# Optimization experiments

Measured on AMD Instinct MI355X. Metric: run time of the kernel, lower is better.

The kernel has to match this reference:

```python
import jax, jax.numpy as jnp
import numpy as np

B, S, D, H, F = 2, 2048, 768, 12, 3072
HD = D // H


def setup_inputs() -> dict:
    key = jax.random.key(0)
    ks = jax.random.split(key, 6)
    g = lambda k, sh, sc: jax.random.normal(k, sh, jnp.float32) * sc
    return {
        "x": g(ks[0], (B, S, D), 1.0),
        "mask": jnp.tril(jnp.ones((1, 1, S, S), dtype=jnp.bool_)),  # causal
        "qkv_w": g(ks[1], (3 * D, D), 0.02),
        "qkv_b": jnp.zeros((3 * D,), jnp.float32),
        "out_w": g(ks[2], (D, D), 0.02),
        "out_b": jnp.zeros((D,), jnp.float32),
        "fc1_w": g(ks[3], (F, D), 0.02),
        "fc1_b": jnp.zeros((F,), jnp.float32),
        "fc2_w": g(ks[4], (D, F), 0.02),
        "fc2_b": jnp.zeros((D,), jnp.float32),
        "ln1_w": jnp.ones((D,), jnp.float32),
        "ln1_b": jnp.zeros((D,), jnp.float32),
        "ln2_w": jnp.ones((D,), jnp.float32),
        "ln2_b": jnp.zeros((D,), jnp.float32),
    }


def _layernorm(x, w, b, eps=1e-5):
    m = x.mean(-1, keepdims=True)
    v = ((x - m) ** 2).mean(-1, keepdims=True)
    return (x - m) * jax.lax.rsqrt(v + eps) * w + b


def reference(x, mask, qkv_w, qkv_b, out_w, out_b, fc1_w, fc1_b, fc2_w, fc2_b,
              ln1_w, ln1_b, ln2_w, ln2_b):
    b, s, d = x.shape
    h = d // HD  # num_heads
    # --- pre-norm multi-head self-attention (dropout = eval/identity) ---
    hx = _layernorm(x, ln1_w, ln1_b)
    qkv = hx @ qkv_w.T + qkv_b                      # [b,s,3d]
    qkv = qkv.reshape(b, s, 3, h, HD).transpose(2, 0, 3, 1, 4)  # [3,b,h,s,hd]
    q, k, v = qkv[0], qkv[1], qkv[2]
    scale = jnp.sqrt(jnp.float32(HD))
    scores = jnp.einsum("bhqd,bhkd->bhqk", q, k) / scale  # [b,h,s,s]
    scores = jnp.where(mask, scores, -jnp.inf)
    attn = jax.nn.softmax(scores, axis=-1)
    o = jnp.einsum("bhqk,bhkd->bhqd", attn, v)      # [b,h,s,hd]
    o = o.transpose(0, 2, 1, 3).reshape(b, s, d)
    x = x + (o @ out_w.T + out_b)
    # --- pre-norm GELU feed-forward ---
    h2 = _layernorm(x, ln2_w, ln2_b)
    ff = jax.nn.gelu(h2 @ fc1_w.T + fc1_b, approximate=False) @ fc2_w.T + fc2_b
    return x + ff
```

## Files before the change

### kernel.cpp

```cpp
#include <hip/hip_runtime.h>
#include <hip/hip_bf16.h>
#include <cstdint>
#include <cstddef>

typedef __bf16 bf16;
typedef unsigned short ushort_t;
typedef __attribute__((ext_vector_type(8))) __bf16 bf16x8;
typedef __attribute__((ext_vector_type(4))) __bf16 bf16x4;
typedef __attribute__((ext_vector_type(4))) float f32x4;

#define NB 2
#define NS 2048
#define ND 768
#define NH 12
#define NF 3072
#define NT (NB * NS)

__device__ __forceinline__ f32x4 mfma16(bf16x8 a, bf16x8 b, f32x4 c) {
  return __builtin_amdgcn_mfma_f32_16x16x32_bf16(a, b, c, 0, 0, 0);
}

__device__ __forceinline__ void gl_lds16(const bf16* g, bf16* l) {
  __builtin_amdgcn_global_load_lds(
      (__attribute__((address_space(1))) void*)(uintptr_t)g,
      (__attribute__((address_space(3))) void*)l,
      16, 0, 0);
}

__device__ __forceinline__ int xcd_swz(int lin, int nwg) {
  const int q = nwg >> 3, r = nwg & 7;
  const int x = lin & 7, i = lin >> 3;
  return (x < r ? x * (q + 1) : r * (q + 1) + (x - r) * q) + i;
}

__device__ __forceinline__ float gelu_fast(float v) {
  const float u = v * (0.7978845608028654f + 0.03567740814f * v * v);
  const float e = exp2f(u * 2.885390081777927f);
  return v - v / (1.f + e);
}

__global__ __launch_bounds__(256) void sniff_kernel(
    const ushort_t* __restrict__ x, int* __restrict__ flag) {
  __shared__ int s[4];
  int bad = 0;
  for (int i = threadIdx.x; i < 4096; i += 256) {
    const int e = (x[i] >> 7) & 0xFF;
    bad |= (e >= 0xC0);
  }
  bad = __any(bad) ? 1 : 0;
  if ((threadIdx.x & 63) == 0) s[threadIdx.x >> 6] = bad;
  __syncthreads();
  if (threadIdx.x == 0) *flag = s[0] | s[1] | s[2] | s[3];
}

struct CvtArgs {
  const void* s[8];
  bf16* d[8];
  int n8[8];
  int total8;
};

__global__ __launch_bounds__(256) void cvt_all(CvtArgs a,
                                               const int* __restrict__ flag) {
  const int isf = *flag;
  const int stride = gridDim.x * 256;
  for (int i = blockIdx.x * 256 + threadIdx.x; i < a.total8; i += stride) {
    int seg = 0, off = i;
    while (off >= a.n8[seg]) { off -= a.n8[seg]; ++seg; }
    bf16x8 o;
    if (isf) {
      const float* s = (const float*)a.s[seg] + (size_t)off * 8;
      const f32x4 f0 = *(const f32x4*)s;
      const f32x4 f1 = *(const f32x4*)(s + 4);
#pragma unroll
      for (int j = 0; j < 4; ++j) {
        o[j] = (bf16)f0[j];
        o[4 + j] = (bf16)f1[j];
      }
    } else {
      o = *((const bf16x8*)a.s[seg] + off);
    }
    *((bf16x8*)a.d[seg] + off) = o;
  }
}

__global__ __launch_bounds__(256) void ln_kernel(
    const void* __restrict__ xv, const void* __restrict__ wv,
    const void* __restrict__ bv, bf16* __restrict__ y,
    const int* __restrict__ flag) {
  const int isf = *flag;
  const int row = blockIdx.x * 4 + (threadIdx.x >> 6);
  const int L = threadIdx.x & 63;
  const float* xf = (const float*)xv;
  const bf16* xh = (const bf16*)xv;
  const float* wf = (const float*)wv;
  const bf16* wh = (const bf16*)wv;
  const float* bf_ = (const float*)bv;
  const bf16* bh = (const bf16*)bv;
  const size_t base = (size_t)row * ND;
  float v[12];
  float s = 0.f, s2 = 0.f;
#pragma unroll
  for (int i = 0; i < 12; ++i) {
    const int c = L + i * 64;
    v[i] = isf ? xf[base + c] : (float)xh[base + c];
    s += v[i];
    s2 += v[i] * v[i];
  }
#pragma unroll
  for (int off = 1; off < 64; off <<= 1) {
    s += __shfl_xor(s, off);
    s2 += __shfl_xor(s2, off);
  }
  const float mean = s * (1.f / 768.f);
  const float var = s2 * (1.f / 768.f) - mean * mean;
  const float rstd = rsqrtf(var + 1e-5f);
  bf16* yr = y + base;
#pragma unroll
  for (int i = 0; i < 12; ++i) {
    const int c = L + i * 64;
    const float ww = isf ? wf[c] : (float)wh[c];
    const float bb = isf ? bf_[c] : (float)bh[c];
    yr[c] = (bf16)((v[i] - mean) * rstd * ww + bb);
  }
}

__global__ __launch_bounds__(256) void vt_kernel(
    const bf16* __restrict__ qkv, bf16* __restrict__ vT) {
  const int bh = blockIdx.y;
  const int b = bh / NH, h = bh % NH;
  const int st = blockIdx.x;
  __shared__ bf16 Vs[64 * 72];
  const int tid = threadIdx.x;
  {
    const int r = tid >> 2, c = (tid & 3) * 16;
    const bf16* src =
        qkv + (size_t)(b * NS + st * 64 + r) * (3 * ND) + 2 * ND + h * 64 + c;
    *(bf16x8*)&Vs[r * 72 + c] = *(const bf16x8*)src;
    *(bf16x8*)&Vs[r * 72 + c + 8] = *(const bf16x8*)(src + 8);
  }
  __syncthreads();
  {
    const int hd = tid >> 2, t0 = (tid & 3) * 16;
    bf16x8 o0, o1;
#pragma unroll
    for (int j = 0; j < 8; ++j) {
      o0[j] = Vs[(t0 + j) * 72 + hd];
      o1[j] = Vs[(t0 + 8 + j) * 72 + hd];
    }
    bf16* dst = vT + ((size_t)bh * 64 + hd) * NS + st * 64 + t0;
    *(bf16x8*)dst = o0;
    *(bf16x8*)(dst + 8) = o1;
  }
}

template <int EPI, int TM>
__global__ __launch_bounds__(256) void gemm_fast(
    const bf16* __restrict__ A, const bf16* __restrict__ Bt,
    const bf16* __restrict__ bias, const void* resid, void* C,
    int N, int K, int row0, const int* __restrict__ flag) {
  constexpr int NBUF = (TM == 64) ? 5 : 3;
  constexpr int LOOK = NBUF - 2;
  constexpr int MT = TM / 32;
  __shared__ bf16 As[NBUF][TM * 32];
  __shared__ bf16 Bs[NBUF][128 * 32];
  int isf = 0;
  if (EPI == 2) {
    isf = *flag;
    asm volatile("" ::"s"(isf));
  }
  const int tid = threadIdx.x;
  const int w = tid >> 6, L = tid & 63;
  const int lg = L >> 4, lc = L & 15;
  const int lgx = (lg ^ ((lc >> 1) & 3)) * 8;
  const int wm = (w >> 1) * (TM / 2), wn = (w & 1) * 64;
  const int nwg = gridDim.x * gridDim.y;
  const int lin = xcd_swz(blockIdx.y * gridDim.x + blockIdx.x, nwg);
  const int bm = lin / gridDim.x, bn = lin % gridDim.x;

  const bf16* Ab = A + (size_t)bm * TM * K;
  const bf16* Bb = Bt + (size_t)bn * 128 * K;

  const int sr = tid >> 2;
  const int sc = ((tid & 3) ^ ((tid >> 3) & 3)) * 8;

  f32x4 acc[MT][4];
#pragma unroll
  for (int i = 0; i < MT; ++i)
#pragma unroll
    for (int j = 0; j < 4; ++j) acc[i][j] = (f32x4){0.f, 0.f, 0.f, 0.f};

#define GF_STAGE(buf, kk)                                                   \
  do {                                                                      \
    gl_lds16(Ab + (size_t)sr * K + (kk) + sc, As[buf] + tid * 8);           \
    if (TM == 128)                                                          \
      gl_lds16(Ab + (size_t)(sr + 64) * K + (kk) + sc,                      \
               As[buf] + 2048 + tid * 8);                                   \
    gl_lds16(Bb + (size_t)sr * K + (kk) + sc, Bs[buf] + tid * 8);           \
    gl_lds16(Bb + (size_t)(sr + 64) * K + (kk) + sc,                        \
             Bs[buf] + 2048 + tid * 8);                                     \
  } while (0)

#define GF_COMP(cb)                                                         \
  do {                                                                      \
    bf16x8 af[MT], bfr[4];                                                  \
    _Pragma("unroll") for (int mt = 0; mt < MT; ++mt) af[mt] =              \
        *(const bf16x8*)&As[cb][(wm + mt * 16 + lc) * 32 + lgx];            \
    _Pragma("unroll") for (int nt = 0; nt < 4; ++nt) bfr[nt] =              \
        *(const bf16x8*)&Bs[cb][(wn + nt * 16 + lc) * 32 + lgx];            \
    _Pragma("unroll") for (int mt = 0; mt < MT; ++mt)                       \
        _Pragma("unroll") for (int nt = 0; nt < 4; ++nt) acc[mt][nt] =      \
            mfma16(af[mt], bfr[nt], acc[mt][nt]);                           \
  } while (0)

  const int nk = K >> 5;
#pragma unroll
  for (int s = 0; s < LOOK; ++s)
    if (s < nk) GF_STAGE(s, s * 32);
  int cur = 0, stg = LOOK;
  int k = 0;
  const int kmain = (nk > LOOK) ? nk - LOOK : 0;
  for (; k < kmain; ++k) {
    GF_STAGE(stg, (k + LOOK) * 32);
    if (TM == 64)
      asm volatile("s_waitcnt vmcnt(9)" ::: "memory");
    else
      asm volatile("s_waitcnt vmcnt(4)" ::: "memory");
    asm volatile("s_barrier" ::: "memory");
    GF_COMP(cur);
    cur = (cur + 1 == NBUF) ? 0 : cur + 1;
    stg = (stg + 1 == NBUF) ? 0 : stg + 1;
  }
  __syncthreads();
  for (; k < nk; ++k) {
    GF_COMP(cur);
    cur = (cur + 1 == NBUF) ? 0 : cur + 1;
  }
#undef GF_STAGE
#undef GF_COMP

  const float* rf = (const float*)resid;
  const bf16* rh = (const bf16*)resid;
  float* Cf = (float*)C;
  bf16* Ch = (bf16*)C;
#pragma unroll
  for (int mt = 0; mt < MT; ++mt) {
#pragma unroll
    for (int nt = 0; nt < 4; ++nt) {
      const int col = bn * 128 + wn + nt * 16 + lc;
      const float bv = (float)bias[col];
#pragma unroll
      for (int r = 0; r < 4; ++r) {
        const int row = bm * TM + wm + mt * 16 + lg * 4 + r;
        float v = acc[mt][nt][r] + bv;
        if (EPI == 1) v = gelu_fast(v);
        const size_t idx = (size_t)(row0 + row) * N + col;
        if (EPI == 2) {
          v += isf ? rf[idx] : (float)rh[idx];
          if (isf) Cf[idx] = v; else Ch[idx] = (bf16)v;
        } else {
          Ch[idx] = (bf16)v;
        }
      }
    }
  }
}

__global__ __launch_bounds__(256) void gemm_qkv(
    const bf16* __restrict__ A, const bf16* __restrict__ Bt,
    const bf16* __restrict__ bias, bf16* __restrict__ qkvout,
    bf16* __restrict__ vT) {
  const int K = ND, N = 3 * ND;
  constexpr int NBUF = 3;
  constexpr int LOOK = 1;
  __shared__ bf16 As[NBUF][128 * 32];
  __shared__ bf16 Bs[NBUF][128 * 32];
  const int tid = threadIdx.x;
  const int w = tid >> 6, L = tid & 63;
  const int lg = L >> 4, lc = L & 15;
  const int lgx = (lg ^ ((lc >> 1) & 3)) * 8;
  const int wm = (w >> 1) * 64, wn = (w & 1) * 64;
  const int nwg = gridDim.x * gridDim.y;
  const int lin = xcd_swz(blockIdx.y * gridDim.x + blockIdx.x, nwg);
  const int bm = lin / gridDim.x, bn = lin % gridDim.x;

  const bf16* Ab = A + (size_t)bm * 128 * K;
  const bf16* Bb = Bt + (size_t)bn * 128 * K;

  const int sr = tid >> 2;
  const int sc = ((tid & 3) ^ ((tid >> 3) & 3)) * 8;

  f32x4 acc[4][4];
#pragma unroll
  for (int i = 0; i < 4; ++i)
#pragma unroll
    for (int j = 0; j < 4; ++j) acc[i][j] = (f32x4){0.f, 0.f, 0.f, 0.f};

#define QKV_STAGE(buf, kk)                                                  \
  do {                                                                      \
    gl_lds16(Ab + (size_t)sr * K + (kk) + sc, As[buf] + tid * 8);           \
    gl_lds16(Ab + (size_t)(sr + 64) * K + (kk) + sc,                        \
             As[buf] + 2048 + tid * 8);                                     \
    gl_lds16(Bb + (size_t)sr * K + (kk) + sc, Bs[buf] + tid * 8);           \
    gl_lds16(Bb + (size_t)(sr + 64) * K + (kk) + sc,                        \
             Bs[buf] + 2048 + tid * 8);                                     \
  } while (0)

#define QKV_COMP(cb)                                                        \
  do {                                                                      \
    bf16x8 af[4], bfr[4];                                                   \
    _Pragma("unroll") for (int mt = 0; mt < 4; ++mt) af[mt] =               \
        *(const bf16x8*)&As[cb][(wm + mt * 16 + lc) * 32 + lgx];            \
    _Pragma("unroll") for (int nt = 0; nt < 4; ++nt) bfr[nt] =              \
        *(const bf16x8*)&Bs[cb][(wn + nt * 16 + lc) * 32 + lgx];            \
    _Pragma("unroll") for (int mt = 0; mt < 4; ++mt)                        \
        _Pragma("unroll") for (int nt = 0; nt < 4; ++nt) acc[mt][nt] =      \
            mfma16(af[mt], bfr[nt], acc[mt][nt]);                           \
  } while (0)

  const int nk = K >> 5;
  QKV_STAGE(0, 0);
  int cur = 0, stg = LOOK;
  int k = 0;
  const int kmain = nk - LOOK;
  for (; k < kmain; ++k) {
    QKV_STAGE(stg, (k + LOOK) * 32);
    asm volatile("s_waitcnt vmcnt(4)" ::: "memory");
    asm volatile("s_barrier" ::: "memory");
    QKV_COMP(cur);
    cur = (cur + 1 == NBUF) ? 0 : cur + 1;
    stg = (stg + 1 == NBUF) ? 0 : stg + 1;
  }
  __syncthreads();
  for (; k < nk; ++k) {
    QKV_COMP(cur);
    cur = (cur + 1 == NBUF) ? 0 : cur + 1;
  }
#undef QKV_STAGE
#undef QKV_COMP

#pragma unroll
  for (int mt = 0; mt < 4; ++mt) {
#pragma unroll
    for (int nt = 0; nt < 4; ++nt) {
      const int col = bn * 128 + wn + nt * 16 + lc;
      const float bv = (float)bias[col];
      if (col < 2 * ND) {
#pragma unroll
        for (int r = 0; r < 4; ++r) {
          const int row = bm * 128 + wm + mt * 16 + lg * 4 + r;
          qkvout[(size_t)row * N + col] = (bf16)(acc[mt][nt][r] + bv);
        }
      } else {
        const int colv = col - 2 * ND;
        const int h_ = colv >> 6, hd = colv & 63;
        bf16x4 pk;
#pragma unroll
        for (int r = 0; r < 4; ++r) pk[r] = (bf16)(acc[mt][nt][r] + bv);
        const int tok0 = bm * 128 + wm + mt * 16 + lg * 4;
        const int b_ = tok0 >> 11, s0 = tok0 & (NS - 1);
        *(bf16x4*)&vT[((size_t)(b_ * NH + h_) * 64 + hd) * NS + s0] = pk;
      }
    }
  }
}

template <int EPI>
__global__ __launch_bounds__(256) void gemm_bt(
    const bf16* __restrict__ A, const void* __restrict__ Bt,
    const void* __restrict__ bias, const void* resid, void* C,
    int N, int K, int row0, const int* __restrict__ flag) {
  __shared__ bf16 As[128 * 32];
  __shared__ bf16 Bs[128 * 32];
  const int isf = *flag;
  const int tid = threadIdx.x;
  const int w = tid >> 6, L = tid & 63;
  const int lg = L >> 4, lc = L & 15;
  const int wm = (w >> 1) * 64, wn = (w & 1) * 64;
  const int nwg = gridDim.x * gridDim.y;
  const int lin = xcd_swz(blockIdx.y * gridDim.x + blockIdx.x, nwg);
  const int bm = lin / gridDim.x, bn = lin % gridDim.x;

  const bf16* Ab = A + (size_t)bm * 128 * K;
  const bf16* Bth = (const bf16*)Bt + (size_t)bn * 128 * K;
  const float* Btf = (const float*)Bt + (size_t)bn * 128 * K;

  const int sr = tid >> 1;
  const int sc = (tid & 1) * 16;

  f32x4 acc[4][4];
#pragma unroll
  for (int i = 0; i < 4; ++i)
#pragma unroll
    for (int j = 0; j < 4; ++j) acc[i][j] = (f32x4){0.f, 0.f, 0.f, 0.f};

  for (int k0 = 0; k0 < K; k0 += 32) {
    const bf16* ap = Ab + (size_t)sr * K + k0 + sc;
    const bf16x8 a0 = *(const bf16x8*)ap;
    const bf16x8 a1 = *(const bf16x8*)(ap + 8);
    bf16x8 b0, b1;
    if (isf) {
      const float* bp = Btf + (size_t)sr * K + k0 + sc;
      const f32x4 f0 = *(const f32x4*)bp;
      const f32x4 f1 = *(const f32x4*)(bp + 4);
      const f32x4 f2 = *(const f32x4*)(bp + 8);
      const f32x4 f3 = *(const f32x4*)(bp + 12);
#pragma unroll
      for (int j = 0; j < 4; ++j) {
        b0[j] = (bf16)f0[j];
        b0[4 + j] = (bf16)f1[j];
        b1[j] = (bf16)f2[j];
        b1[4 + j] = (bf16)f3[j];
      }
    } else {
      const bf16* bp = Bth + (size_t)sr * K + k0 + sc;
      b0 = *(const bf16x8*)bp;
      b1 = *(const bf16x8*)(bp + 8);
    }
    __syncthreads();
    *(bf16x8*)&As[sr * 32 + sc] = a0;
    *(bf16x8*)&As[sr * 32 + sc + 8] = a1;
    *(bf16x8*)&Bs[sr * 32 + sc] = b0;
    *(bf16x8*)&Bs[sr * 32 + sc + 8] = b1;
    __syncthreads();

    bf16x8 af[4], bfr[4];
#pragma unroll
    for (int mt = 0; mt < 4; ++mt)
      af[mt] = *(const bf16x8*)&As[(wm + mt * 16 + lc) * 32 + lg * 8];
#pragma unroll
    for (int nt = 0; nt < 4; ++nt)
      bfr[nt] = *(const bf16x8*)&Bs[(wn + nt * 16 + lc) * 32 + lg * 8];
#pragma unroll
    for (int mt = 0; mt < 4; ++mt)
#pragma unroll
      for (int nt = 0; nt < 4; ++nt)
        acc[mt][nt] = mfma16(af[mt], bfr[nt], acc[mt][nt]);
  }

  const float* biasf = (const float*)bias;
  const bf16* biash = (const bf16*)bias;
  const float* rf = (const float*)resid;
  const bf16* rh = (const bf16*)resid;
  float* Cf = (float*)C;
  bf16* Ch = (bf16*)C;
#pragma unroll
  for (int mt = 0; mt < 4; ++mt) {
#pragma unroll
    for (int nt = 0; nt < 4; ++nt) {
      const int col = bn * 128 + wn + nt * 16 + lc;
      const float bv = isf ? biasf[col] : (float)biash[col];
#pragma unroll
      for (int r = 0; r < 4; ++r) {
        const int row = bm * 128 + wm + mt * 16 + lg * 4 + r;
        float v = acc[mt][nt][r] + bv;
        if (EPI == 1) v = gelu_fast(v);
        const size_t idx = (size_t)(row0 + row) * N + col;
        if (EPI == 2) {
          v += isf ? rf[idx] : (float)rh[idx];
          if (isf) Cf[idx] = v; else Ch[idx] = (bf16)v;
        } else {
          Ch[idx] = (bf16)v;
        }
      }
    }
  }
}

__global__ __launch_bounds__(128) void flash_attn_v7(
    const bf16* __restrict__ qkv, const bf16* __restrict__ vT,
    bf16* __restrict__ o) {
  const int nwg = gridDim.x * gridDim.y;
  const int lin = xcd_swz(blockIdx.y * gridDim.x + blockIdx.x, nwg);
  const int xcd = lin / 96;
  const int i96 = lin % 96;
  const int bl = i96 >> 5;
  const int j = i96 & 31;
  const int bh = xcd * 3 + bl;
  const int b = bh / NH, h = bh % NH;
  int qt;
  if (bl == 0) qt = j;
  else if (bl == 1) qt = (j + 16) & 31;
  else qt = (j < 16) ? (31 - 2 * j) : (62 - 2 * j);
  const int q0 = qt * 64;
  const int tid = threadIdx.x;
  const int w = tid >> 6, L = tid & 63;
  const int lg = L >> 4, lc = L & 15;

  __shared__ bf16 Ks[2][64 * 72];
  __shared__ bf16 Vts[2][64 * 72];
  __shared__ bf16 Ps[2][32 * 72];

  const float QSCALE = 0.18033688011112042f;
  bf16x8 qf[2][2];
#pragma unroll
  for (int m = 0; m < 2; ++m) {
    const size_t tokq = (size_t)(b * NS + q0 + w * 32 + m * 16 + lc);
    const bf16* qp = qkv + tokq * (3 * ND) + h * 64 + lg * 8;
    const bf16x8 q0r = *(const bf16x8*)qp;
    const bf16x8 q1r = *(const bf16x8*)(qp + 32);
#pragma unroll
    for (int jj = 0; jj < 8; ++jj) {
      qf[m][0][jj] = (bf16)((float)q0r[jj] * QSCALE);
      qf[m][1][jj] = (bf16)((float)q1r[jj] * QSCALE);
    }
  }

  const int kr = tid >> 1, kc = (tid & 1) * 32;
  const bf16* kbase =
      qkv + (size_t)(b * NS + kr) * (3 * ND) + ND + h * 64 + kc;
  const bf16* vbase = vT + ((size_t)bh * 64 + kr) * NS + kc;

  f32x4 oacc[2][4];
#pragma unroll
  for (int m = 0; m < 2; ++m)
#pragma unroll
    for (int nt = 0; nt < 4; ++nt) oacc[m][nt] = (f32x4){0.f, 0.f, 0.f, 0.f};
  float lacc[2] = {0.f, 0.f};

  const int nkt = qt + 1;

  bf16x8 kreg[4], vreg[4];
#pragma unroll
  for (int p = 0; p < 4; ++p) {
    kreg[p] = *(const bf16x8*)(kbase + p * 8);
    vreg[p] = *(const bf16x8*)(vbase + p * 8);
  }
#pragma unroll
  for (int p = 0; p < 4; ++p) {
    *(bf16x8*)&Ks[0][kr * 72 + kc + p * 8] = kreg[p];
    *(bf16x8*)&Vts[0][kr * 72 + kc + p * 8] = vreg[p];
  }

  for (int kt = 0; kt < nkt; ++kt) {
    __syncthreads();
    const int cur = kt & 1;

    if (kt + 1 < nkt) {
      const bf16* kn = kbase + (size_t)(kt + 1) * 64 * (3 * ND);
      const bf16* vn = vbase + (size_t)(kt + 1) * 64;
#pragma unroll
      for (int p = 0; p < 4; ++p) {
        kreg[p] = *(const bf16x8*)(kn + p * 8);
        vreg[p] = *(const bf16x8*)(vn + p * 8);
      }
    }

    f32x4 s[2][4];
    __builtin_amdgcn_s_setprio(1);
#pragma unroll
    for (int nt = 0; nt < 4; ++nt) {
      const bf16x8 kb0 =
          *(const bf16x8*)&Ks[cur][(nt * 16 + lc) * 72 + lg * 8];
      const bf16x8 kb1 =
          *(const bf16x8*)&Ks[cur][(nt * 16 + lc) * 72 + 32 + lg * 8];
#pragma unroll
      for (int m = 0; m < 2; ++m) {
        f32x4 z = (f32x4){0.f, 0.f, 0.f, 0.f};
        s[m][nt] = mfma16(kb0, qf[m][0], z);
        s[m][nt] = mfma16(kb1, qf[m][1], s[m][nt]);
      }
    }
    __builtin_amdgcn_s_setprio(0);
    if (kt == nkt - 1) {
#pragma unroll
      for (int m = 0; m < 2; ++m)
#pragma unroll
        for (int nt = 0; nt < 4; ++nt)
#pragma unroll
          for (int r = 0; r < 4; ++r) {
            const int kv = nt * 16 + lg * 4 + r;
            const int qrow = w * 32 + m * 16 + lc;
            if (kv > qrow) s[m][nt][r] = -1.0e30f;
          }
    }
#pragma unroll
    for (int m = 0; m < 2; ++m)
#pragma unroll
      for (int nt = 0; nt < 4; ++nt) {
        bf16x4 pk;
#pragma unroll
        for (int r = 0; r < 4; ++r) {
          const float p = exp2f(fminf(s[m][nt][r], 20.f));
          lacc[m] += p;
          pk[r] = (bf16)p;
        }
        *(bf16x4*)&Ps[w][(m * 16 + lc) * 72 + nt * 16 + lg * 4] = pk;
      }
    bf16x8 pa[2][2];
#pragma unroll
    for (int m = 0; m < 2; ++m) {
      pa[m][0] = *(const bf16x8*)&Ps[w][(m * 16 + lc) * 72 + lg * 8];
      pa[m][1] = *(const bf16x8*)&Ps[w][(m * 16 + lc) * 72 + 32 + lg * 8];
    }

    if (kt + 1 < nkt) {
      const int nxt = cur ^ 1;
#pragma unroll
      for (int p = 0; p < 4; ++p) {
        *(bf16x8*)&Ks[nxt][kr * 72 + kc + p * 8] = kreg[p];
        *(bf16x8*)&Vts[nxt][kr * 72 + kc + p * 8] = vreg[p];
      }
    }

    __builtin_amdgcn_s_setprio(1);
#pragma unroll
    for (int nt = 0; nt < 4; ++nt) {
      const bf16x8 v0 =
          *(const bf16x8*)&Vts[cur][(nt * 16 + lc) * 72 + lg * 8];
      const bf16x8 v1 =
          *(const bf16x8*)&Vts[cur][(nt * 16 + lc) * 72 + 32 + lg * 8];
#pragma unroll
      for (int m = 0; m < 2; ++m) {
        oacc[m][nt] = mfma16(pa[m][0], v0, oacc[m][nt]);
        oacc[m][nt] = mfma16(pa[m][1], v1, oacc[m][nt]);
      }
    }
    __builtin_amdgcn_s_setprio(0);
  }

#pragma unroll
  for (int m = 0; m < 2; ++m) {
    lacc[m] += __shfl_xor(lacc[m], 16);
    lacc[m] += __shfl_xor(lacc[m], 32);
  }
  float lr[2][4];
#pragma unroll
  for (int m = 0; m < 2; ++m)
#pragma unroll
    for (int r = 0; r < 4; ++r) lr[m][r] = __shfl(lacc[m], lg * 4 + r);

#pragma unroll
  for (int m = 0; m < 2; ++m)
#pragma unroll
    for (int nt = 0; nt < 4; ++nt)
#pragma unroll
      for (int r = 0; r < 4; ++r) {
        const int qrow = q0 + w * 32 + m * 16 + lg * 4 + r;
        const float val = oacc[m][nt][r] / lr[m][r];
        o[(size_t)(b * NS + qrow) * ND + h * 64 + nt * 16 + lc] = (bf16)val;
      }
}

__global__ __launch_bounds__(256) void flash_attn_v1(
    const bf16* __restrict__ qkv, bf16* __restrict__ o) {
  const int bh = blockIdx.y;
  const int b = bh / NH, h = bh % NH;
  const int qt = gridDim.x - 1 - blockIdx.x;
  const int q0 = qt * 64;
  const int tid = threadIdx.x;
  const int w = tid >> 6, L = tid & 63;
  const int lg = L >> 4, lc = L & 15;

  __shared__ bf16 Ks[64 * 72];
  __shared__ bf16 Vts[64 * 72];
  __shared__ bf16 Ps[4][16 * 72];

  const float QSCALE = 0.18033688011112042f;
  const size_t tokq = (size_t)(b * NS + q0 + w * 16 + lc);
  const bf16* qp = qkv + tokq * (3 * ND) + h * 64 + lg * 8;
  const bf16x8 qr0 = *(const bf16x8*)qp;
  const bf16x8 qr1 = *(const bf16x8*)(qp + 32);
  bf16x8 qf0, qf1;
#pragma unroll
  for (int j = 0; j < 8; ++j) {
    qf0[j] = (bf16)((float)qr0[j] * QSCALE);
    qf1[j] = (bf16)((float)qr1[j] * QSCALE);
  }

  f32x4 oacc[4];
#pragma unroll
  for (int nt = 0; nt < 4; ++nt) oacc[nt] = (f32x4){0.f, 0.f, 0.f, 0.f};
  float lacc[4] = {0.f, 0.f, 0.f, 0.f};

  for (int kt = 0; kt <= qt; ++kt) {
    __syncthreads();
#pragma unroll
    for (int p = 0; p < 2; ++p) {
      const int r = (p * 256 + tid) >> 3;
      const int c = (tid & 7) * 8;
      const bf16* kp =
          qkv + (size_t)(b * NS + kt * 64 + r) * (3 * ND) + ND + h * 64 + c;
      const bf16x8 k8 = *(const bf16x8*)kp;
      *(bf16x8*)&Ks[r * 72 + c] = k8;
      const bf16x8 v8 = *(const bf16x8*)(kp + ND);
#pragma unroll
      for (int j = 0; j < 8; ++j) Vts[(c + j) * 72 + r] = v8[j];
    }
    __syncthreads();

    f32x4 s[4];
#pragma unroll
    for (int nt = 0; nt < 4; ++nt) {
      const bf16x8 b0 = *(const bf16x8*)&Ks[(nt * 16 + lc) * 72 + lg * 8];
      const bf16x8 b1 = *(const bf16x8*)&Ks[(nt * 16 + lc) * 72 + 32 + lg * 8];
      f32x4 z = (f32x4){0.f, 0.f, 0.f, 0.f};
      s[nt] = mfma16(qf0, b0, z);
      s[nt] = mfma16(qf1, b1, s[nt]);
    }
    if (kt == qt) {
#pragma unroll
      for (int nt = 0; nt < 4; ++nt)
#pragma unroll
        for (int r = 0; r < 4; ++r) {
          const int qrow = w * 16 + lg * 4 + r;
          const int kcol = nt * 16 + lc;
          if (kcol > qrow) s[nt][r] = -1.0e30f;
        }
    }
#pragma unroll
    for (int nt = 0; nt < 4; ++nt)
#pragma unroll
      for (int r = 0; r < 4; ++r) {
        const float p = exp2f(fminf(s[nt][r], 20.f));
        lacc[r] += p;
        Ps[w][(lg * 4 + r) * 72 + nt * 16 + lc] = (bf16)p;
      }
    __syncthreads();

    const bf16x8 p0 = *(const bf16x8*)&Ps[w][lc * 72 + lg * 8];
    const bf16x8 p1 = *(const bf16x8*)&Ps[w][lc * 72 + 32 + lg * 8];
#pragma unroll
    for (int nt = 0; nt < 4; ++nt) {
      const bf16x8 v0 = *(const bf16x8*)&Vts[(nt * 16 + lc) * 72 + lg * 8];
      const bf16x8 v1 = *(const bf16x8*)&Vts[(nt * 16 + lc) * 72 + 32 + lg * 8];
      oacc[nt] = mfma16(p0, v0, oacc[nt]);
      oacc[nt] = mfma16(p1, v1, oacc[nt]);
    }
  }

#pragma unroll
  for (int msk = 1; msk < 16; msk <<= 1)
#pragma unroll
    for (int r = 0; r < 4; ++r) lacc[r] += __shfl_xor(lacc[r], msk);

#pragma unroll
  for (int nt = 0; nt < 4; ++nt)
#pragma unroll
    for (int r = 0; r < 4; ++r) {
      const int qrow = q0 + w * 16 + lg * 4 + r;
      const float val = oacc[nt][r] / lacc[r];
      o[(size_t)(b * NS + qrow) * ND + h * 64 + nt * 16 + lc] = (bf16)val;
    }
}

extern "C" void kernel_launch(void* const* d_in, const int* in_sizes, int n_in,
                              void* d_out, int out_size, void* d_ws,
                              size_t ws_size, hipStream_t stream) {
  const void* x = d_in[0];
  const void* qkv_w = d_in[2];
  const void* qkv_b = d_in[3];
  const void* out_w = d_in[4];
  const void* out_b = d_in[5];
  const void* fc1_w = d_in[6];
  const void* fc1_b = d_in[7];
  const void* fc2_w = d_in[8];
  const void* fc2_b = d_in[9];
  const void* ln1_w = d_in[10];
  const void* ln1_b = d_in[11];
  const void* ln2_w = d_in[12];
  const void* ln2_b = d_in[13];
  (void)in_sizes; (void)n_in; (void)out_size;

  char* ws = (char*)d_ws;
  int* flag = (int*)ws;

  sniff_kernel<<<dim3(1), 256, 0, stream>>>((const ushort_t*)x, flag);

  const size_t T1 = 58210048, T2 = 51918592, T3 = 45627136, T4 = 39335680;

  if (ws_size >= T2) {
    bf16* wq = (bf16*)(ws + 256);
    bf16* wo = wq + 1769472;
    bf16* w1 = wo + 589824;
    bf16* w2 = w1 + 2359296;
    bf16* bq = w2 + 2359296;
    bf16* bo = bq + 2304;
    bf16* b1 = bo + 768;
    bf16* b2 = b1 + 3072;
    bf16* slotA = b2 + 768;
    bf16* vT = slotA + (size_t)NT * ND;
    bf16* slotB = vT + (size_t)NT * ND;
    bf16* hx = slotA, *oat = slotA, *h2 = slotA;
    bf16* qkv = slotB;

    CvtArgs ca;
    ca.s[0] = qkv_w; ca.d[0] = wq; ca.n8[0] = 1769472 / 8;
    ca.s[1] = out_w; ca.d[1] = wo; ca.n8[1] = 589824 / 8;
    ca.s[2] = fc1_w; ca.d[2] = w1; ca.n8[2] = 2359296 / 8;
    ca.s[3] = fc2_w; ca.d[3] = w2; ca.n8[3] = 2359296 / 8;
    ca.s[4] = qkv_b; ca.d[4] = bq; ca.n8[4] = 2304 / 8;
    ca.s[5] = out_b; ca.d[5] = bo; ca.n8[5] = 768 / 8;
    ca.s[6] = fc1_b; ca.d[6] = b1; ca.n8[6] = 3072 / 8;
    ca.s[7] = fc2_b; ca.d[7] = b2; ca.n8[7] = 768 / 8;
    ca.total8 = (1769472 + 589824 + 2359296 + 2359296 + 2304 + 768 + 3072 +
                 768) / 8;
    cvt_all<<<dim3(880), 256, 0, stream>>>(ca, flag);

    ln_kernel<<<dim3(NT / 4), 256, 0, stream>>>(x, ln1_w, ln1_b, hx, flag);
    gemm_qkv<<<dim3(18, 32), 256, 0, stream>>>(hx, wq, bq, qkv, vT);
    flash_attn_v7<<<dim3(NS / 64, NB * NH), 128, 0, stream>>>(qkv, vT, oat);
    gemm_fast<2, 64><<<dim3(6, 64), 256, 0, stream>>>(
        oat, wo, bo, x, d_out, ND, ND, 0, flag);
    ln_kernel<<<dim3(NT / 4), 256, 0, stream>>>(d_out, ln2_w, ln2_b, h2, flag);
    if (ws_size >= T1) {
      bf16* ff1 = slotB;
      gemm_fast<1, 128><<<dim3(24, 32), 256, 0, stream>>>(
          h2, w1, b1, nullptr, ff1, NF, ND, 0, flag);
      gemm_fast<2, 64><<<dim3(6, 64), 256, 0, stream>>>(
          ff1, w2, b2, d_out, d_out, ND, NF, 0, flag);
    } else {
      bf16* ff1c = slotB;
      for (int c = 0; c < 2; ++c) {
        gemm_fast<1, 128><<<dim3(24, 16), 256, 0, stream>>>(
            h2 + (size_t)c * 2048 * ND, w1, b1, nullptr, ff1c, NF, ND, 0, flag);
        gemm_fast<2, 64><<<dim3(6, 32), 256, 0, stream>>>(
            ff1c, w2, b2, d_out, d_out, ND, NF, c * 2048, flag);
      }
    }
  } else if (ws_size >= T4) {
    bf16* wq = (bf16*)(ws + 256);
    bf16* wo = wq + 1769472;
    bf16* w1 = wo + 589824;
    bf16* w2 = w1 + 2359296;
    bf16* bq = w2 + 2359296;
    bf16* bo = bq + 2304;
    bf16* b1 = bo + 768;
    bf16* b2 = b1 + 3072;
    bf16* slotA = b2 + 768;
    bf16* slotB = slotA + (size_t)NT * ND;
    bf16* hx = slotA, *oat = slotA, *h2 = slotA;
    bf16* qkv = slotB;

    CvtArgs ca;
    ca.s[0] = qkv_w; ca.d[0] = wq; ca.n8[0] = 1769472 / 8;
    ca.s[1] = out_w; ca.d[1] = wo; ca.n8[1] = 589824 / 8;
    ca.s[2] = fc1_w; ca.d[2] = w1; ca.n8[2] = 2359296 / 8;
    ca.s[3] = fc2_w; ca.d[3] = w2; ca.n8[3] = 2359296 / 8;
    ca.s[4] = qkv_b; ca.d[4] = bq; ca.n8[4] = 2304 / 8;
    ca.s[5] = out_b; ca.d[5] = bo; ca.n8[5] = 768 / 8;
    ca.s[6] = fc1_b; ca.d[6] = b1; ca.n8[6] = 3072 / 8;
    ca.s[7] = fc2_b; ca.d[7] = b2; ca.n8[7] = 768 / 8;
    ca.total8 = (1769472 + 589824 + 2359296 + 2359296 + 2304 + 768 + 3072 +
                 768) / 8;
    cvt_all<<<dim3(880), 256, 0, stream>>>(ca, flag);

    ln_kernel<<<dim3(NT / 4), 256, 0, stream>>>(x, ln1_w, ln1_b, hx, flag);
    gemm_fast<0, 128><<<dim3(18, 32), 256, 0, stream>>>(
        hx, wq, bq, nullptr, qkv, 3 * ND, ND, 0, flag);
    flash_attn_v1<<<dim3(NS / 64, NB * NH), 256, 0, stream>>>(qkv, oat);
    gemm_fast<2, 64><<<dim3(6, 64), 256, 0, stream>>>(
        oat, wo, bo, x, d_out, ND, ND, 0, flag);
    ln_kernel<<<dim3(NT / 4), 256, 0, stream>>>(d_out, ln2_w, ln2_b, h2, flag);
    if (ws_size >= T3) {
      bf16* ff1 = slotB;
      gemm_fast<1, 128><<<dim3(24, 32), 256, 0, stream>>>(
          h2, w1, b1, nullptr, ff1, NF, ND, 0, flag);
      gemm_fast<2, 64><<<dim3(6, 64), 256, 0, stream>>>(
          ff1, w2, b2, d_out, d_out, ND, NF, 0, flag);
    } else {
      bf16* ff1c = slotB;
      for (int c = 0; c < 2; ++c) {
        gemm_fast<1, 128><<<dim3(24, 16), 256, 0, stream>>>(
            h2 + (size_t)c * 2048 * ND, w1, b1, nullptr, ff1c, NF, ND, 0, flag);
        gemm_fast<2, 64><<<dim3(6, 32), 256, 0, stream>>>(
            ff1c, w2, b2, d_out, d_out, ND, NF, c * 2048, flag);
      }
    }
  } else {
    const size_t szTD = (size_t)NT * ND * sizeof(bf16);
    bf16* slotA = (bf16*)(ws + 256);
    bf16* qkv = (bf16*)(ws + 256 + szTD);
    bf16* hx = slotA, *oat = slotA, *h2 = slotA;
    bf16* ff1c = qkv;

    ln_kernel<<<dim3(NT / 4), 256, 0, stream>>>(x, ln1_w, ln1_b, hx, flag);
    gemm_bt<0><<<dim3(18, 32), 256, 0, stream>>>(
        hx, qkv_w, qkv_b, nullptr, qkv, 3 * ND, ND, 0, flag);
    flash_attn_v1<<<dim3(NS / 64, NB * NH), 256, 0, stream>>>(qkv, oat);
    gemm_bt<2><<<dim3(6, 32), 256, 0, stream>>>(
        oat, out_w, out_b, x, d_out, ND, ND, 0, flag);
    ln_kernel<<<dim3(NT / 4), 256, 0, stream>>>(d_out, ln2_w, ln2_b, h2, flag);
    for (int c = 0; c < 4; ++c) {
      gemm_bt<1><<<dim3(24, 8), 256, 0, stream>>>(
          h2 + (size_t)c * 1024 * ND, fc1_w, fc1_b, nullptr, ff1c, NF, ND, 0,
          flag);
      gemm_bt<2><<<dim3(6, 8), 256, 0, stream>>>(
          ff1c, fc2_w, fc2_b, d_out, d_out, ND, NF, c * 1024, flag);
    }
  }
}
```

Before: 336.0 us.

## Split long causal query tiles across two workgroups and combine partial attention outputs

Adds a split-KV flash attention kernel: for query tiles 17-31 the key range is divided into two halves processed by separate workgroups, which write unnormalized fp32 partial outputs and row sums to workspace. A small combine kernel then sums the partials and normalizes. This balances per-workgroup work under the causal mask and raises parallelism (47 instead of 32 blocks per head). The cost is an extra kernel launch and extra fp32 traffic for the partials. It relies on the scores staying small, since there is no running max and exp2 is clamped at 20.

```diff
diff --git a/kernel.cpp b/kernel.cpp
--- a/kernel.cpp
+++ b/kernel.cpp
@@ -464,6 +464,216 @@
         }
       }
     }
+  }
+}
+
+__global__ __launch_bounds__(128) void flash_attn_sp(
+    const bf16* __restrict__ qkv, const bf16* __restrict__ vT,
+    bf16* __restrict__ o, float* __restrict__ po, float* __restrict__ pl) {
+  const int nwg = gridDim.x * gridDim.y;
+  const int lin = xcd_swz(blockIdx.y * gridDim.x + blockIdx.x, nwg);
+  const int bh = lin / 47;
+  const int c = lin % 47;
+  const int b = bh / NH, h = bh % NH;
+  int qt, kt_lo, kt_hi, direct, cc = 0;
+  if (c == 0) {
+    qt = 16; kt_lo = 0; kt_hi = 16; direct = 1;
+  } else if (c <= 30) {
+    qt = 31 - ((c - 1) >> 1);
+    const int hh = (qt + 1) >> 1;
+    cc = (c - 1) & 1;
+    if (cc) { kt_lo = hh; kt_hi = qt; }
+    else    { kt_lo = 0;  kt_hi = hh - 1; }
+    direct = 0;
+  } else {
+    qt = 46 - c; kt_lo = 0; kt_hi = qt; direct = 1;
+  }
+  const int q0 = qt * 64;
+  const int tid = threadIdx.x;
+  const int w = tid >> 6, L = tid & 63;
+  const int lg = L >> 4, lc = L & 15;
+
+  __shared__ bf16 Ks[64 * 72];
+  __shared__ bf16 Vts[64 * 72];
+  __shared__ bf16 Ps[2][32 * 72];
+
+  const float QSCALE = 0.18033688011112042f;
+  bf16x8 qf[2][2];
+#pragma unroll
+  for (int m = 0; m < 2; ++m) {
+    const size_t tokq = (size_t)(b * NS + q0 + w * 32 + m * 16 + lc);
+    const bf16* qp = qkv + tokq * (3 * ND) + h * 64 + lg * 8;
+    const bf16x8 q0r = *(const bf16x8*)qp;
+    const bf16x8 q1r = *(const bf16x8*)(qp + 32);
+#pragma unroll
+    for (int jj = 0; jj < 8; ++jj) {
+      qf[m][0][jj] = (bf16)((float)q0r[jj] * QSCALE);
+      qf[m][1][jj] = (bf16)((float)q1r[jj] * QSCALE);
+    }
+  }
+
+  const int kr = tid >> 1, kc = (tid & 1) * 32;
+  const bf16* kbase =
+      qkv + (size_t)(b * NS + kr) * (3 * ND) + ND + h * 64 + kc;
+  const bf16* vbase = vT + ((size_t)bh * 64 + kr) * NS + kc;
+
+  f32x4 oacc[2][4];
+#pragma unroll
+  for (int m = 0; m < 2; ++m)
+#pragma unroll
+    for (int nt = 0; nt < 4; ++nt) oacc[m][nt] = (f32x4){0.f, 0.f, 0.f, 0.f};
+  float lacc[2] = {0.f, 0.f};
+
+  bf16x8 kreg[4], vreg[4];
+  {
+    const bf16* kn = kbase + (size_t)kt_lo * 64 * (3 * ND);
+    const bf16* vn = vbase + (size_t)kt_lo * 64;
+#pragma unroll
+    for (int p = 0; p < 4; ++p) {
+      kreg[p] = *(const bf16x8*)(kn + p * 8);
+      vreg[p] = *(const bf16x8*)(vn + p * 8);
+    }
+  }
+
+  for (int kt = kt_lo; kt <= kt_hi; ++kt) {
+    __syncthreads();
+#pragma unroll
+    for (int p = 0; p < 4; ++p) {
+      *(bf16x8*)&Ks[kr * 72 + kc + p * 8] = kreg[p];
+      *(bf16x8*)&Vts[kr * 72 + kc + p * 8] = vreg[p];
+    }
+    __syncthreads();
+
+    if (kt < kt_hi) {
+      const bf16* kn = kbase + (size_t)(kt + 1) * 64 * (3 * ND);
+      const bf16* vn = vbase + (size_t)(kt + 1) * 64;
+#pragma unroll
+      for (int p = 0; p < 4; ++p) {
+        kreg[p] = *(const bf16x8*)(kn + p * 8);
+        vreg[p] = *(const bf16x8*)(vn + p * 8);
+      }
+    }
+
+    f32x4 s[2][4];
+    __builtin_amdgcn_s_setprio(1);
+#pragma unroll
+    for (int nt = 0; nt < 4; ++nt) {
+      const bf16x8 kb0 = *(const bf16x8*)&Ks[(nt * 16 + lc) * 72 + lg * 8];
+      const bf16x8 kb1 =
+          *(const bf16x8*)&Ks[(nt * 16 + lc) * 72 + 32 + lg * 8];
+#pragma unroll
+      for (int m = 0; m < 2; ++m) {
+        f32x4 z = (f32x4){0.f, 0.f, 0.f, 0.f};
+        s[m][nt] = mfma16(kb0, qf[m][0], z);
+        s[m][nt] = mfma16(kb1, qf[m][1], s[m][nt]);
+      }
+    }
+    __builtin_amdgcn_s_setprio(0);
+    if (kt == qt) {
+#pragma unroll
+      for (int m = 0; m < 2; ++m)
+#pragma unroll
+        for (int nt = 0; nt < 4; ++nt)
+#pragma unroll
+          for (int r = 0; r < 4; ++r) {
+            const int kv = nt * 16 + lg * 4 + r;
+            const int qrow = w * 32 + m * 16 + lc;
+            if (kv > qrow) s[m][nt][r] = -1.0e30f;
+          }
+    }
+#pragma unroll
+    for (int m = 0; m < 2; ++m)
+#pragma unroll
+      for (int nt = 0; nt < 4; ++nt) {
+        bf16x4 pk;
+#pragma unroll
+        for (int r = 0; r < 4; ++r) {
+          const float p = exp2f(fminf(s[m][nt][r], 20.f));
+          lacc[m] += p;
+          pk[r] = (bf16)p;
+        }
+        *(bf16x4*)&Ps[w][(m * 16 + lc) * 72 + nt * 16 + lg * 4] = pk;
+      }
+    bf16x8 pa[2][2];
+#pragma unroll
+    for (int m = 0; m < 2; ++m) {
+      pa[m][0] = *(const bf16x8*)&Ps[w][(m * 16 + lc) * 72 + lg * 8];
+      pa[m][1] = *(const bf16x8*)&Ps[w][(m * 16 + lc) * 72 + 32 + lg * 8];
+    }
+    __builtin_amdgcn_s_setprio(1);
+#pragma unroll
+    for (int nt = 0; nt < 4; ++nt) {
+      const bf16x8 v0 = *(const bf16x8*)&Vts[(nt * 16 + lc) * 72 + lg * 8];
+      const bf16x8 v1 =
+          *(const bf16x8*)&Vts[(nt * 16 + lc) * 72 + 32 + lg * 8];
+#pragma unroll
+      for (int m = 0; m < 2; ++m) {
+        oacc[m][nt] = mfma16(pa[m][0], v0, oacc[m][nt]);
+        oacc[m][nt] = mfma16(pa[m][1], v1, oacc[m][nt]);
+      }
+    }
+    __builtin_amdgcn_s_setprio(0);
+  }
+
+#pragma unroll
+  for (int m = 0; m < 2; ++m) {
+    lacc[m] += __shfl_xor(lacc[m], 16);
+    lacc[m] += __shfl_xor(lacc[m], 32);
+  }
+
+  if (direct) {
+    float lr[2][4];
+#pragma unroll
+    for (int m = 0; m < 2; ++m)
+#pragma unroll
+      for (int r = 0; r < 4; ++r) lr[m][r] = __shfl(lacc[m], lg * 4 + r);
+#pragma unroll
+    for (int m = 0; m < 2; ++m)
+#pragma unroll
+      for (int nt = 0; nt < 4; ++nt)
+#pragma unroll
+        for (int r = 0; r < 4; ++r) {
+          const int qrow = q0 + w * 32 + m * 16 + lg * 4 + r;
+          const float val = oacc[m][nt][r] / lr[m][r];
+          o[(size_t)(b * NS + qrow) * ND + h * 64 + nt * 16 + lc] =
+              (bf16)val;
+        }
+  } else {
+    const int slot = qt - 17;
+    float* pob = po + (((size_t)(bh * 15 + slot)) * 2 + cc) * 4096;
+#pragma unroll
+    for (int m = 0; m < 2; ++m)
+#pragma unroll
+      for (int nt = 0; nt < 4; ++nt)
+#pragma unroll
+        for (int r = 0; r < 4; ++r) {
+          const int row = w * 32 + m * 16 + lg * 4 + r;
+          const int col = nt * 16 + lc;
+          pob[row * 64 + col] = oacc[m][nt][r];
+        }
+    if (L < 16) {
+      float* plb = pl + ((bh * 15 + slot) * 2 + cc) * 64;
+      plb[w * 32 + L] = lacc[0];
+      plb[w * 32 + 16 + L] = lacc[1];
+    }
+  }
+}
+
+__global__ __launch_bounds__(256) void attn_combine(
+    const float* __restrict__ po, const float* __restrict__ pl,
+    bf16* __restrict__ o) {
+  const int slot = blockIdx.x;
+  const int bh = blockIdx.y;
+  const int qt = slot + 17;
+  const int b = bh / NH, h = bh % NH;
+  const float* poA = po + ((size_t)(bh * 15 + slot)) * 2 * 4096;
+  const float* poB = poA + 4096;
+  const float* plA = pl + (bh * 15 + slot) * 2 * 64;
+  const float* plB = plA + 64;
+  for (int e = threadIdx.x; e < 4096; e += 256) {
+    const int q = e >> 6, hd = e & 63;
+    const float val = (poA[e] + poB[e]) / (plA[q] + plB[q]);
+    o[(size_t)(b * NS + qt * 64 + q) * ND + h * 64 + hd] = (bf16)val;
   }
 }
 
@@ -783,6 +993,9 @@
     bf16* slotB = vT + (size_t)NT * ND;
     bf16* hx = slotA, *oat = slotA, *h2 = slotA;
     bf16* qkv = slotB;
+    float* po = (float*)(ws + 45627136);
+    float* pl = po + (size_t)24 * 15 * 2 * 4096;
+    const bool sp = ws_size >= T1;
 
     CvtArgs ca;
     ca.s[0] = qkv_w; ca.d[0] = wq; ca.n8[0] = 1769472 / 8;
@@ -799,7 +1012,12 @@
 
     ln_kernel<<<dim3(NT / 4), 256, 0, stream>>>(x, ln1_w, ln1_b, hx, flag);
     gemm_qkv<<<dim3(18, 32), 256, 0, stream>>>(hx, wq, bq, qkv, vT);
-    flash_attn_v7<<<dim3(NS / 64, NB * NH), 128, 0, stream>>>(qkv, vT, oat);
+    if (sp) {
+      flash_attn_sp<<<dim3(47, 24), 128, 0, stream>>>(qkv, vT, oat, po, pl);
+      attn_combine<<<dim3(15, 24), 256, 0, stream>>>(po, pl, oat);
+    } else {
+      flash_attn_v7<<<dim3(NS / 64, NB * NH), 128, 0, stream>>>(qkv, vT, oat);
+    }
     gemm_fast<2, 64><<<dim3(6, 64), 256, 0, stream>>>(
         oat, wo, bo, x, d_out, ND, ND, 0, flag);
     ln_kernel<<<dim3(NT / 4), 256, 0, stream>>>(d_out, ln2_w, ln2_b, h2, flag);
```

Measured after the change: 325.5 us. 1.03x faster.
